# Kernel tuning notes

Measured on AMD Instinct MI355X. Metric: run time of the kernel, lower is better.

Reference implementation:

```python
import jax, jax.numpy as jnp
import numpy as np

EPS = 1e-8  # torch CosineSimilarity default eps

def setup_inputs() -> dict:
    key = jax.random.key(0)
    kv, kt, k1, k2, k3, k4 = jax.random.split(key, 6)
    B, S = 16, 1024
    VD, TD, H = 1024, 768, 512
    visual_features = jax.random.normal(kv, (B, S, VD), dtype=jnp.float32)
    text_features = jax.random.normal(kt, (B, S, TD), dtype=jnp.float32)
    # nn.Linear params: weight [out, in], bias [out]
    Wv = jax.random.normal(k1, (H, VD), dtype=jnp.float32) * (1.0 / np.sqrt(VD))
    bv = jax.random.normal(k2, (H,), dtype=jnp.float32) * 0.01
    Wt = jax.random.normal(k3, (H, TD), dtype=jnp.float32) * (1.0 / np.sqrt(TD))
    bt = jax.random.normal(k4, (H,), dtype=jnp.float32) * 0.01
    return {"visual_features": visual_features, "text_features": text_features,
            "Wv": Wv, "bv": bv, "Wt": Wt, "bt": bt}

def reference(visual_features, text_features, Wv, bv, Wt, bt):
    # Linear projections
    v = jnp.einsum('bsd,hd->bsh', visual_features, Wv) + bv  # [B,S,H]
    t = jnp.einsum('bsd,hd->bsh', text_features, Wt) + bt    # [B,S,H]
    # Cosine similarity matrix via normalized batched GEMM
    # (algebraically equal to broadcasting CosineSimilarity over (B,S,S,H))
    dots = jnp.einsum('bih,bjh->bij', v, t)                   # [B,S,S]
    vn = jnp.linalg.norm(v, axis=-1)                          # [B,S]
    tn = jnp.linalg.norm(t, axis=-1)                          # [B,S]
    denom = jnp.maximum(vn[:, :, None] * tn[:, None, :], EPS)
    return dots / denom
```

## Files before the change

### kernel.cpp

```cpp
#include <hip/hip_runtime.h>
#include <hip/hip_bf16.h>

typedef __bf16 bf16x8 __attribute__((ext_vector_type(8)));
typedef __bf16 bf16x4 __attribute__((ext_vector_type(4)));
typedef float  f32x4  __attribute__((ext_vector_type(4)));

#define MFMA16(a, b, c) __builtin_amdgcn_mfma_f32_16x16x32_bf16((a), (b), (c), 0, 0, 0)

#define BATCH 16
#define SEQ   1024
#define VD    1024
#define TD    768
#define HDIM  512
#define MROWS (BATCH * SEQ)

typedef __attribute__((address_space(1))) const unsigned int gas_uint;
typedef __attribute__((address_space(3))) unsigned int las_uint;

__device__ __forceinline__ void async_copy16(const void* g, void* l) {
    __builtin_amdgcn_global_load_lds((gas_uint*)g, (las_uint*)l, 16, 0, 0);
}

template <int K>
__global__ __launch_bounds__(256) void proj_kernel(const float* __restrict__ X,
                                                   const float* __restrict__ W,
                                                   const float* __restrict__ bias,
                                                   __bf16* __restrict__ out) {
    __shared__ __bf16 As[128 * 32];
    __shared__ __bf16 Bs[128 * 32];

    const int n0   = blockIdx.x * 128;
    const int m0   = blockIdx.y * 128;
    const int tid  = threadIdx.x;
    const int lane = tid & 63;
    const int wave = tid >> 6;
    const int wr   = wave >> 1;
    const int wc   = wave & 1;
    const int fr   = lane & 15;
    const int fq   = lane >> 4;

    f32x4 acc[4][4] = {};

    for (int kk = 0; kk < K; kk += 32) {
#pragma unroll
        for (int it = 0; it < 4; ++it) {
            const int f   = tid + it * 256;
            const int row = f >> 3;
            const int c4  = f & 7;
            const float4 xa = *reinterpret_cast<const float4*>(&X[(size_t)(m0 + row) * K + kk + c4 * 4]);
            bf16x4 pa = {(__bf16)xa.x, (__bf16)xa.y, (__bf16)xa.z, (__bf16)xa.w};
            *reinterpret_cast<bf16x4*>(&As[row * 32 + c4 * 4]) = pa;
            const float4 xb = *reinterpret_cast<const float4*>(&W[(size_t)(n0 + row) * K + kk + c4 * 4]);
            bf16x4 pb = {(__bf16)xb.x, (__bf16)xb.y, (__bf16)xb.z, (__bf16)xb.w};
            *reinterpret_cast<bf16x4*>(&Bs[row * 32 + c4 * 4]) = pb;
        }
        __syncthreads();

        bf16x8 a[4], b[4];
#pragma unroll
        for (int t = 0; t < 4; ++t) {
            a[t] = *reinterpret_cast<const bf16x8*>(&As[(wr * 64 + t * 16 + fr) * 32 + fq * 8]);
            b[t] = *reinterpret_cast<const bf16x8*>(&Bs[(wc * 64 + t * 16 + fr) * 32 + fq * 8]);
        }
#pragma unroll
        for (int tm = 0; tm < 4; ++tm)
#pragma unroll
            for (int tn = 0; tn < 4; ++tn)
                acc[tm][tn] = MFMA16(a[tm], b[tn], acc[tm][tn]);
        __syncthreads();
    }

#pragma unroll
    for (int tn = 0; tn < 4; ++tn) {
        const int col  = n0 + wc * 64 + tn * 16 + fr;
        const float bc = bias[col];
#pragma unroll
        for (int tm = 0; tm < 4; ++tm) {
            const int rowb = m0 + wr * 64 + tm * 16 + fq * 4;
#pragma unroll
            for (int r = 0; r < 4; ++r) {
                out[(size_t)(rowb + r) * HDIM + col] = (__bf16)(acc[tm][tn][r] + bc);
            }
        }
    }
}

__global__ __launch_bounds__(256) void norm_kernel(const __bf16* __restrict__ v,
                                                   const __bf16* __restrict__ t,
                                                   float* __restrict__ vn,
                                                   float* __restrict__ tn) {
    const int g    = blockIdx.x * 4 + (threadIdx.x >> 6);
    const int lane = threadIdx.x & 63;
    const __bf16* src = v;
    float* dst = vn;
    int row = g;
    if (g >= MROWS) { src = t; dst = tn; row = g - MROWS; }
    const bf16x8 x = *reinterpret_cast<const bf16x8*>(&src[(size_t)row * HDIM + lane * 8]);
    float s = 0.f;
#pragma unroll
    for (int j = 0; j < 8; ++j) {
        const float f = (float)x[j];
        s = fmaf(f, f, s);
    }
#pragma unroll
    for (int off = 32; off > 0; off >>= 1) s += __shfl_down(s, off);
    if (lane == 0) dst[row] = sqrtf(s);
}

__global__ __launch_bounds__(256) void dots_kernel(const __bf16* __restrict__ v,
                                                   const __bf16* __restrict__ t,
                                                   const float* __restrict__ vn,
                                                   const float* __restrict__ tn,
                                                   float* __restrict__ out) {
    __shared__ __bf16 As[128 * 32];
    __shared__ __bf16 Bs[128 * 32];

    const int b  = blockIdx.z;
    const int j0 = blockIdx.x * 128;
    const int i0 = blockIdx.y * 128;
    const __bf16* vb = v + (size_t)b * SEQ * HDIM;
    const __bf16* tb = t + (size_t)b * SEQ * HDIM;

    const int tid  = threadIdx.x;
    const int lane = tid & 63;
    const int wave = tid >> 6;
    const int wr   = wave >> 1;
    const int wc   = wave & 1;
    const int fr   = lane & 15;
    const int fq   = lane >> 4;

    f32x4 acc[4][4] = {};

    for (int kk = 0; kk < HDIM; kk += 32) {
#pragma unroll
        for (int s = 0; s < 2; ++s) {
            const int c    = (wave * 2 + s) * 64 + lane;
            const int row  = c >> 2;
            const int part = c & 3;
            async_copy16(&vb[(size_t)(i0 + row) * HDIM + kk + part * 8],
                         &As[(wave * 2 + s) * 512]);
            async_copy16(&tb[(size_t)(j0 + row) * HDIM + kk + part * 8],
                         &Bs[(wave * 2 + s) * 512]);
        }
        __syncthreads();

        bf16x8 a[4], bfr[4];
#pragma unroll
        for (int t_ = 0; t_ < 4; ++t_) {
            a[t_]   = *reinterpret_cast<const bf16x8*>(&As[(wr * 64 + t_ * 16 + fr) * 32 + fq * 8]);
            bfr[t_] = *reinterpret_cast<const bf16x8*>(&Bs[(wc * 64 + t_ * 16 + fr) * 32 + fq * 8]);
        }
#pragma unroll
        for (int tm = 0; tm < 4; ++tm)
#pragma unroll
            for (int tn_ = 0; tn_ < 4; ++tn_)
                acc[tm][tn_] = MFMA16(a[tm], bfr[tn_], acc[tm][tn_]);
        __syncthreads();
    }

    float vr[16];
#pragma unroll
    for (int tm = 0; tm < 4; ++tm)
#pragma unroll
        for (int r = 0; r < 4; ++r)
            vr[tm * 4 + r] = vn[b * SEQ + i0 + wr * 64 + tm * 16 + fq * 4 + r];

    float* outb = out + ((size_t)b << 20);
#pragma unroll
    for (int tn_ = 0; tn_ < 4; ++tn_) {
        const int j    = j0 + wc * 64 + tn_ * 16 + fr;
        const float tj = tn[b * SEQ + j];
#pragma unroll
        for (int tm = 0; tm < 4; ++tm) {
            const int ib = i0 + wr * 64 + tm * 16 + fq * 4;
#pragma unroll
            for (int r = 0; r < 4; ++r) {
                const float denom = fmaxf(vr[tm * 4 + r] * tj, 1e-8f);
                outb[(size_t)(ib + r) * SEQ + j] = acc[tm][tn_][r] * __builtin_amdgcn_rcpf(denom);
            }
        }
    }
}

extern "C" void kernel_launch(void* const* d_in, const int* in_sizes, int n_in,
                              void* d_out, int out_size, void* d_ws, size_t ws_size,
                              hipStream_t stream) {
    const float* Xv = (const float*)d_in[0];
    const float* Xt = (const float*)d_in[1];
    const float* Wv = (const float*)d_in[2];
    const float* bv = (const float*)d_in[3];
    const float* Wt = (const float*)d_in[4];
    const float* bt = (const float*)d_in[5];
    float* out = (float*)d_out;

    char* ws = (char*)d_ws;
    __bf16* v  = (__bf16*)ws;
    __bf16* t  = (__bf16*)(ws + (size_t)MROWS * HDIM * 2);
    float*  vn = (float*)(ws + (size_t)2 * MROWS * HDIM * 2);
    float*  tn = (float*)(ws + (size_t)2 * MROWS * HDIM * 2 + (size_t)MROWS * 4);

    proj_kernel<VD><<<dim3(4, 128), 256, 0, stream>>>(Xv, Wv, bv, v);
    proj_kernel<TD><<<dim3(4, 128), 256, 0, stream>>>(Xt, Wt, bt, t);

    norm_kernel<<<8192, 256, 0, stream>>>(v, t, vn, tn);

    dots_kernel<<<dim3(8, 8, BATCH), 256, 0, stream>>>(v, t, vn, tn, out);
}
```

Baseline: 275.0 us.

## Merge projection GEMMs into one launch with register-prefetched double-buffered LDS

The two projection kernels are merged into a single launch, with the z-dimension selecting the visual or text input, so both fill the GPU together. The K-loop now double-buffers the shared tiles. The next fp32 tile is loaded into registers before the MFMAs on the current tile, and is converted and stored to the other buffer afterwards, leaving one barrier per iteration. This aims to hide global-load latency and reduce launch and tail costs, in exchange for higher register and LDS use. K becomes a runtime value, which may cost some unrolling.

New measurement: 267.3 us. 1.03x faster.

```diff
diff --git a/kernel.cpp b/kernel.cpp
--- a/kernel.cpp
+++ b/kernel.cpp
@@ -21,13 +21,19 @@
     __builtin_amdgcn_global_load_lds((gas_uint*)g, (las_uint*)l, 16, 0, 0);
 }
 
-template <int K>
-__global__ __launch_bounds__(256) void proj_kernel(const float* __restrict__ X,
-                                                   const float* __restrict__ W,
-                                                   const float* __restrict__ bias,
-                                                   __bf16* __restrict__ out) {
-    __shared__ __bf16 As[128 * 32];
-    __shared__ __bf16 Bs[128 * 32];
+__global__ __launch_bounds__(256) void proj_dual_kernel(
+    const float* __restrict__ Xv, const float* __restrict__ Wv, const float* __restrict__ bv_,
+    const float* __restrict__ Xt, const float* __restrict__ Wt, const float* __restrict__ bt_,
+    __bf16* __restrict__ vout, __bf16* __restrict__ tout)
+{
+    const float *X, *W, *bias;
+    __bf16* out;
+    int K;
+    if (blockIdx.z == 0) { X = Xv; W = Wv; bias = bv_; out = vout; K = VD; }
+    else                 { X = Xt; W = Wt; bias = bt_; out = tout; K = TD; }
+
+    __shared__ __bf16 As[2][128 * 32];
+    __shared__ __bf16 Bs[2][128 * 32];
 
     const int n0   = blockIdx.x * 128;
     const int m0   = blockIdx.y * 128;
@@ -39,35 +45,81 @@
     const int fr   = lane & 15;
     const int fq   = lane >> 4;
 
+    int srow[4], sc4[4];
+#pragma unroll
+    for (int it = 0; it < 4; ++it) {
+        const int f = tid + it * 256;
+        srow[it] = f >> 3;
+        sc4[it]  = f & 7;
+    }
+
+    float4 ra[4], rb[4];
+
+#pragma unroll
+    for (int it = 0; it < 4; ++it) {
+        ra[it] = *reinterpret_cast<const float4*>(&X[(size_t)(m0 + srow[it]) * K + sc4[it] * 4]);
+        rb[it] = *reinterpret_cast<const float4*>(&W[(size_t)(n0 + srow[it]) * K + sc4[it] * 4]);
+    }
+#pragma unroll
+    for (int it = 0; it < 4; ++it) {
+        bf16x4 pa = {(__bf16)ra[it].x, (__bf16)ra[it].y, (__bf16)ra[it].z, (__bf16)ra[it].w};
+        *reinterpret_cast<bf16x4*>(&As[0][srow[it] * 32 + sc4[it] * 4]) = pa;
+        bf16x4 pb = {(__bf16)rb[it].x, (__bf16)rb[it].y, (__bf16)rb[it].z, (__bf16)rb[it].w};
+        *reinterpret_cast<bf16x4*>(&Bs[0][srow[it] * 32 + sc4[it] * 4]) = pb;
+    }
+    __syncthreads();
+
     f32x4 acc[4][4] = {};
-
-    for (int kk = 0; kk < K; kk += 32) {
+    const int nk = K >> 5;
+
+    for (int ki = 0; ki < nk - 1; ++ki) {
+        const int kk = (ki + 1) << 5;
 #pragma unroll
         for (int it = 0; it < 4; ++it) {
-            const int f   = tid + it * 256;
-            const int row = f >> 3;
-            const int c4  = f & 7;
-            const float4 xa = *reinterpret_cast<const float4*>(&X[(size_t)(m0 + row) * K + kk + c4 * 4]);
-            bf16x4 pa = {(__bf16)xa.x, (__bf16)xa.y, (__bf16)xa.z, (__bf16)xa.w};
-            *reinterpret_cast<bf16x4*>(&As[row * 32 + c4 * 4]) = pa;
-            const float4 xb = *reinterpret_cast<const float4*>(&W[(size_t)(n0 + row) * K + kk + c4 * 4]);
-            bf16x4 pb = {(__bf16)xb.x, (__bf16)xb.y, (__bf16)xb.z, (__bf16)xb.w};
-            *reinterpret_cast<bf16x4*>(&Bs[row * 32 + c4 * 4]) = pb;
-        }
-        __syncthreads();
-
+            ra[it] = *reinterpret_cast<const float4*>(&X[(size_t)(m0 + srow[it]) * K + kk + sc4[it] * 4]);
+            rb[it] = *reinterpret_cast<const float4*>(&W[(size_t)(n0 + srow[it]) * K + kk + sc4[it] * 4]);
+        }
+
+        const __bf16* Ab = As[ki & 1];
+        const __bf16* Bb = Bs[ki & 1];
         bf16x8 a[4], b[4];
 #pragma unroll
-        for (int t = 0; t < 4; ++t) {
-            a[t] = *reinterpret_cast<const bf16x8*>(&As[(wr * 64 + t * 16 + fr) * 32 + fq * 8]);
-            b[t] = *reinterpret_cast<const bf16x8*>(&Bs[(wc * 64 + t * 16 + fr) * 32 + fq * 8]);
+        for (int t_ = 0; t_ < 4; ++t_) {
+            a[t_] = *reinterpret_cast<const bf16x8*>(&Ab[(wr * 64 + t_ * 16 + fr) * 32 + fq * 8]);
+            b[t_] = *reinterpret_cast<const bf16x8*>(&Bb[(wc * 64 + t_ * 16 + fr) * 32 + fq * 8]);
         }
 #pragma unroll
         for (int tm = 0; tm < 4; ++tm)
 #pragma unroll
             for (int tn = 0; tn < 4; ++tn)
                 acc[tm][tn] = MFMA16(a[tm], b[tn], acc[tm][tn]);
+
+        __bf16* Aw = As[(ki + 1) & 1];
+        __bf16* Bw = Bs[(ki + 1) & 1];
+#pragma unroll
+        for (int it = 0; it < 4; ++it) {
+            bf16x4 pa = {(__bf16)ra[it].x, (__bf16)ra[it].y, (__bf16)ra[it].z, (__bf16)ra[it].w};
+            *reinterpret_cast<bf16x4*>(&Aw[srow[it] * 32 + sc4[it] * 4]) = pa;
+            bf16x4 pb = {(__bf16)rb[it].x, (__bf16)rb[it].y, (__bf16)rb[it].z, (__bf16)rb[it].w};
+            *reinterpret_cast<bf16x4*>(&Bw[srow[it] * 32 + sc4[it] * 4]) = pb;
+        }
         __syncthreads();
+    }
+
+    {
+        const __bf16* Ab = As[(nk - 1) & 1];
+        const __bf16* Bb = Bs[(nk - 1) & 1];
+        bf16x8 a[4], b[4];
+#pragma unroll
+        for (int t_ = 0; t_ < 4; ++t_) {
+            a[t_] = *reinterpret_cast<const bf16x8*>(&Ab[(wr * 64 + t_ * 16 + fr) * 32 + fq * 8]);
+            b[t_] = *reinterpret_cast<const bf16x8*>(&Bb[(wc * 64 + t_ * 16 + fr) * 32 + fq * 8]);
+        }
+#pragma unroll
+        for (int tm = 0; tm < 4; ++tm)
+#pragma unroll
+            for (int tn = 0; tn < 4; ++tn)
+                acc[tm][tn] = MFMA16(a[tm], b[tn], acc[tm][tn]);
     }
 
 #pragma unroll
@@ -199,8 +251,7 @@
     float*  vn = (float*)(ws + (size_t)2 * MROWS * HDIM * 2);
     float*  tn = (float*)(ws + (size_t)2 * MROWS * HDIM * 2 + (size_t)MROWS * 4);
 
-    proj_kernel<VD><<<dim3(4, 128), 256, 0, stream>>>(Xv, Wv, bv, v);
-    proj_kernel<TD><<<dim3(4, 128), 256, 0, stream>>>(Xt, Wt, bt, t);
+    proj_dual_kernel<<<dim3(4, 128, 2), 256, 0, stream>>>(Xv, Wv, bv, Xt, Wt, bt, v, t);
 
     norm_kernel<<<8192, 256, 0, stream>>>(v, t, vn, tn);
 
```

## Fuse row norms into projection epilogue and restructure projection GEMM

Applied to the files above, without the earlier changes.

Pre-converts the weights to bf16 in a separate kernel. The two projection launches become one kernel: each 512-thread block computes a 128-row by full-512-column tile, reads the weight fragments directly from global memory, and double-buffers the activation tile in padded LDS. The squared row norms are accumulated in the projection epilogue via shuffles and atomics, which removes the separate norm kernel; the dots kernel now takes the sqrt of the product of squared norms. This adds a memset and atomic traffic, and gives up the LDS reuse of the weight tile.

Result: no change. 279.4 us (+1.6%).

```diff
diff --git a/kernel.cpp b/kernel.cpp
--- a/kernel.cpp
+++ b/kernel.cpp
@@ -21,96 +21,136 @@
     __builtin_amdgcn_global_load_lds((gas_uint*)g, (las_uint*)l, 16, 0, 0);
 }
 
-template <int K>
-__global__ __launch_bounds__(256) void proj_kernel(const float* __restrict__ X,
-                                                   const float* __restrict__ W,
-                                                   const float* __restrict__ bias,
-                                                   __bf16* __restrict__ out) {
-    __shared__ __bf16 As[128 * 32];
-    __shared__ __bf16 Bs[128 * 32];
-
-    const int n0   = blockIdx.x * 128;
-    const int m0   = blockIdx.y * 128;
+__global__ __launch_bounds__(256) void wconv_kernel(const float* __restrict__ Wv,
+                                                    const float* __restrict__ Wt,
+                                                    __bf16* __restrict__ Wbv,
+                                                    __bf16* __restrict__ Wbt) {
+    const int NV = (HDIM * VD) / 4;
+    const int NT = (HDIM * TD) / 4;
+    int i = blockIdx.x * 256 + threadIdx.x;
+    const float* src;
+    __bf16* dst;
+    if (i < NV) { src = Wv; dst = Wbv; }
+    else        { i -= NV; if (i >= NT) return; src = Wt; dst = Wbt; }
+    const float4 x = reinterpret_cast<const float4*>(src)[i];
+    bf16x4 p = {(__bf16)x.x, (__bf16)x.y, (__bf16)x.z, (__bf16)x.w};
+    reinterpret_cast<bf16x4*>(dst)[i] = p;
+}
+
+#define APAD 40
+
+__global__ __launch_bounds__(512, 2) void proj_kernel(
+    const float* __restrict__ Xv, const __bf16* __restrict__ Wbv, const float* __restrict__ bv_,
+    const float* __restrict__ Xt, const __bf16* __restrict__ Wbt, const float* __restrict__ bt_,
+    __bf16* __restrict__ vout, __bf16* __restrict__ tout,
+    float* __restrict__ vn2, float* __restrict__ tn2)
+{
+    const float* X; const __bf16* Wb; const float* bias; __bf16* out; float* n2; int K;
+    if (blockIdx.y == 0) { X = Xv; Wb = Wbv; bias = bv_; out = vout; n2 = vn2; K = VD; }
+    else                 { X = Xt; Wb = Wbt; bias = bt_; out = tout; n2 = tn2; K = TD; }
+
+    __shared__ __bf16 As[2][128 * APAD];
+
+    const int m0   = blockIdx.x * 128;
     const int tid  = threadIdx.x;
     const int lane = tid & 63;
     const int wave = tid >> 6;
-    const int wr   = wave >> 1;
-    const int wc   = wave & 1;
+    const int wr   = wave & 1;
+    const int wc   = wave >> 1;
     const int fr   = lane & 15;
     const int fq   = lane >> 4;
 
-    f32x4 acc[4][4] = {};
-
-    for (int kk = 0; kk < K; kk += 32) {
-#pragma unroll
-        for (int it = 0; it < 4; ++it) {
-            const int f   = tid + it * 256;
-            const int row = f >> 3;
-            const int c4  = f & 7;
-            const float4 xa = *reinterpret_cast<const float4*>(&X[(size_t)(m0 + row) * K + kk + c4 * 4]);
-            bf16x4 pa = {(__bf16)xa.x, (__bf16)xa.y, (__bf16)xa.z, (__bf16)xa.w};
-            *reinterpret_cast<bf16x4*>(&As[row * 32 + c4 * 4]) = pa;
-            const float4 xb = *reinterpret_cast<const float4*>(&W[(size_t)(n0 + row) * K + kk + c4 * 4]);
-            bf16x4 pb = {(__bf16)xb.x, (__bf16)xb.y, (__bf16)xb.z, (__bf16)xb.w};
-            *reinterpret_cast<bf16x4*>(&Bs[row * 32 + c4 * 4]) = pb;
-        }
-        __syncthreads();
-
-        bf16x8 a[4], b[4];
-#pragma unroll
-        for (int t = 0; t < 4; ++t) {
-            a[t] = *reinterpret_cast<const bf16x8*>(&As[(wr * 64 + t * 16 + fr) * 32 + fq * 8]);
-            b[t] = *reinterpret_cast<const bf16x8*>(&Bs[(wc * 64 + t * 16 + fr) * 32 + fq * 8]);
-        }
+    int srow[2], sc4[2];
+#pragma unroll
+    for (int it = 0; it < 2; ++it) {
+        const int f = tid + it * 512;
+        srow[it] = f >> 3;
+        sc4[it]  = f & 7;
+    }
+
+    const __bf16* wbase = Wb + (size_t)(wc * 128 + fr) * K + fq * 8;
+
+    f32x4 acc[4][8] = {};
+
+    float4 ra[2];
+#pragma unroll
+    for (int it = 0; it < 2; ++it)
+        ra[it] = *reinterpret_cast<const float4*>(&X[(size_t)(m0 + srow[it]) * K + sc4[it] * 4]);
+#pragma unroll
+    for (int it = 0; it < 2; ++it) {
+        bf16x4 p = {(__bf16)ra[it].x, (__bf16)ra[it].y, (__bf16)ra[it].z, (__bf16)ra[it].w};
+        *reinterpret_cast<bf16x4*>(&As[0][srow[it] * APAD + sc4[it] * 4]) = p;
+    }
+    __syncthreads();
+
+    const int nk = K >> 5;
+    for (int ki = 0; ki < nk; ++ki) {
+        const int kk = ki << 5;
+        const bool more = (ki + 1) < nk;
+        if (more) {
+#pragma unroll
+            for (int it = 0; it < 2; ++it)
+                ra[it] = *reinterpret_cast<const float4*>(&X[(size_t)(m0 + srow[it]) * K + kk + 32 + sc4[it] * 4]);
+        }
+
+        bf16x8 b[8];
+#pragma unroll
+        for (int tn = 0; tn < 8; ++tn)
+            b[tn] = *reinterpret_cast<const bf16x8*>(wbase + (size_t)tn * 16 * K + kk);
+
+        const __bf16* Ab = As[ki & 1];
+        bf16x8 a[4];
 #pragma unroll
         for (int tm = 0; tm < 4; ++tm)
-#pragma unroll
-            for (int tn = 0; tn < 4; ++tn)
+            a[tm] = *reinterpret_cast<const bf16x8*>(&Ab[(wr * 64 + tm * 16 + fr) * APAD + fq * 8]);
+
+#pragma unroll
+        for (int tm = 0; tm < 4; ++tm)
+#pragma unroll
+            for (int tn = 0; tn < 8; ++tn)
                 acc[tm][tn] = MFMA16(a[tm], b[tn], acc[tm][tn]);
-        __syncthreads();
-    }
-
-#pragma unroll
-    for (int tn = 0; tn < 4; ++tn) {
-        const int col  = n0 + wc * 64 + tn * 16 + fr;
-        const float bc = bias[col];
-#pragma unroll
-        for (int tm = 0; tm < 4; ++tm) {
-            const int rowb = m0 + wr * 64 + tm * 16 + fq * 4;
-#pragma unroll
-            for (int r = 0; r < 4; ++r) {
-                out[(size_t)(rowb + r) * HDIM + col] = (__bf16)(acc[tm][tn][r] + bc);
+
+        if (more) {
+            __bf16* Aw = As[(ki + 1) & 1];
+#pragma unroll
+            for (int it = 0; it < 2; ++it) {
+                bf16x4 p = {(__bf16)ra[it].x, (__bf16)ra[it].y, (__bf16)ra[it].z, (__bf16)ra[it].w};
+                *reinterpret_cast<bf16x4*>(&Aw[srow[it] * APAD + sc4[it] * 4]) = p;
             }
-        }
-    }
-}
-
-__global__ __launch_bounds__(256) void norm_kernel(const __bf16* __restrict__ v,
-                                                   const __bf16* __restrict__ t,
-                                                   float* __restrict__ vn,
-                                                   float* __restrict__ tn) {
-    const int g    = blockIdx.x * 4 + (threadIdx.x >> 6);
-    const int lane = threadIdx.x & 63;
-    const __bf16* src = v;
-    float* dst = vn;
-    int row = g;
-    if (g >= MROWS) { src = t; dst = tn; row = g - MROWS; }
-    const bf16x8 x = *reinterpret_cast<const bf16x8*>(&src[(size_t)row * HDIM + lane * 8]);
-    float s = 0.f;
-#pragma unroll
-    for (int j = 0; j < 8; ++j) {
-        const float f = (float)x[j];
-        s = fmaf(f, f, s);
-    }
-#pragma unroll
-    for (int off = 32; off > 0; off >>= 1) s += __shfl_down(s, off);
-    if (lane == 0) dst[row] = sqrtf(s);
+            __syncthreads();
+        }
+    }
+
+    float bc[8];
+#pragma unroll
+    for (int tn = 0; tn < 8; ++tn)
+        bc[tn] = bias[wc * 128 + tn * 16 + fr];
+
+#pragma unroll
+    for (int tm = 0; tm < 4; ++tm) {
+        const int rowb = m0 + wr * 64 + tm * 16 + fq * 4;
+#pragma unroll
+        for (int r = 0; r < 4; ++r) {
+            float s = 0.f;
+#pragma unroll
+            for (int tn = 0; tn < 8; ++tn) {
+                const float e = acc[tm][tn][r] + bc[tn];
+                out[(size_t)(rowb + r) * HDIM + wc * 128 + tn * 16 + fr] = (__bf16)e;
+                s = fmaf(e, e, s);
+            }
+            s += __shfl_xor(s, 1);
+            s += __shfl_xor(s, 2);
+            s += __shfl_xor(s, 4);
+            s += __shfl_xor(s, 8);
+            if (fr == 0) atomicAdd(&n2[rowb + r], s);
+        }
+    }
 }
 
 __global__ __launch_bounds__(256) void dots_kernel(const __bf16* __restrict__ v,
                                                    const __bf16* __restrict__ t,
-                                                   const float* __restrict__ vn,
-                                                   const float* __restrict__ tn,
+                                                   const float* __restrict__ vn2,
+                                                   const float* __restrict__ tn2,
                                                    float* __restrict__ out) {
     __shared__ __bf16 As[128 * 32];
     __shared__ __bf16 Bs[128 * 32];
@@ -158,24 +198,24 @@
         __syncthreads();
     }
 
-    float vr[16];
+    float vr2[16];
 #pragma unroll
     for (int tm = 0; tm < 4; ++tm)
 #pragma unroll
         for (int r = 0; r < 4; ++r)
-            vr[tm * 4 + r] = vn[b * SEQ + i0 + wr * 64 + tm * 16 + fq * 4 + r];
+            vr2[tm * 4 + r] = vn2[b * SEQ + i0 + wr * 64 + tm * 16 + fq * 4 + r];
 
     float* outb = out + ((size_t)b << 20);
 #pragma unroll
     for (int tn_ = 0; tn_ < 4; ++tn_) {
-        const int j    = j0 + wc * 64 + tn_ * 16 + fr;
-        const float tj = tn[b * SEQ + j];
+        const int j     = j0 + wc * 64 + tn_ * 16 + fr;
+        const float tj2 = tn2[b * SEQ + j];
 #pragma unroll
         for (int tm = 0; tm < 4; ++tm) {
             const int ib = i0 + wr * 64 + tm * 16 + fq * 4;
 #pragma unroll
             for (int r = 0; r < 4; ++r) {
-                const float denom = fmaxf(vr[tm * 4 + r] * tj, 1e-8f);
+                const float denom = fmaxf(sqrtf(vr2[tm * 4 + r] * tj2), 1e-8f);
                 outb[(size_t)(ib + r) * SEQ + j] = acc[tm][tn_][r] * __builtin_amdgcn_rcpf(denom);
             }
         }
@@ -194,15 +234,19 @@
     float* out = (float*)d_out;
 
     char* ws = (char*)d_ws;
-    __bf16* v  = (__bf16*)ws;
-    __bf16* t  = (__bf16*)(ws + (size_t)MROWS * HDIM * 2);
-    float*  vn = (float*)(ws + (size_t)2 * MROWS * HDIM * 2);
-    float*  tn = (float*)(ws + (size_t)2 * MROWS * HDIM * 2 + (size_t)MROWS * 4);
-
-    proj_kernel<VD><<<dim3(4, 128), 256, 0, stream>>>(Xv, Wv, bv, v);
-    proj_kernel<TD><<<dim3(4, 128), 256, 0, stream>>>(Xt, Wt, bt, t);
-
-    norm_kernel<<<8192, 256, 0, stream>>>(v, t, vn, tn);
-
-    dots_kernel<<<dim3(8, 8, BATCH), 256, 0, stream>>>(v, t, vn, tn, out);
-}
+    size_t off = 0;
+    __bf16* v   = (__bf16*)(ws + off); off += (size_t)MROWS * HDIM * 2;
+    __bf16* t   = (__bf16*)(ws + off); off += (size_t)MROWS * HDIM * 2;
+    __bf16* Wbv = (__bf16*)(ws + off); off += (size_t)HDIM * VD * 2;
+    __bf16* Wbt = (__bf16*)(ws + off); off += (size_t)HDIM * TD * 2;
+    float*  vn2 = (float*)(ws + off);  off += (size_t)MROWS * 4;
+    float*  tn2 = (float*)(ws + off);  off += (size_t)MROWS * 4;
+
+    hipMemsetAsync(vn2, 0, (size_t)2 * MROWS * 4, stream);
+
+    wconv_kernel<<<896, 256, 0, stream>>>(Wv, Wt, Wbv, Wbt);
+
+    proj_kernel<<<dim3(128, 2), 512, 0, stream>>>(Xv, Wbv, bv, Xt, Wbt, bt, v, t, vn2, tn2);
+
+    dots_kernel<<<dim3(8, 8, BATCH), 256, 0, stream>>>(v, t, vn2, tn2, out);
+}
```
